# Performance work log

Measured on AMD Instinct MI355X. Metric: run time of the kernel, lower is better.

The kernel has to match this reference:

```python
import jax, jax.numpy as jnp
import numpy as np

SIGMA = 1.0
KSIZE = 5
WEAK = 75.0
STRONG = 255.0
LOW_T = 0.00392
HIGH_T = 0.15

# scipy.signal.gaussian(M, std): unnormalized gaussian window
_n = np.arange(KSIZE, dtype=np.float32) - (KSIZE - 1) / 2.0
_g = np.exp(-0.5 * (_n / SIGMA) ** 2).astype(np.float32)
GAUSS_H = jnp.asarray(_g.reshape(1, 1, 1, KSIZE))  # horizontal 1xK
GAUSS_V = jnp.asarray(_g.reshape(1, 1, KSIZE, 1))  # vertical Kx1

_sobel = np.array([[1, 0, -1], [2, 0, -2], [1, 0, -1]], dtype=np.float32)
SOBEL_H = jnp.asarray(_sobel.reshape(1, 1, 3, 3))
SOBEL_V = jnp.asarray(_sobel.T.reshape(1, 1, 3, 3))

_f0 = np.array([[0, 0, 0], [0, 1, -1], [0, 0, 0]], np.float32)
_f45 = np.array([[0, 0, 0], [0, 1, 0], [0, 0, -1]], np.float32)
_f90 = np.array([[0, 0, 0], [0, 1, 0], [0, -1, 0]], np.float32)
_f135 = np.array([[0, 0, 0], [0, 1, 0], [-1, 0, 0]], np.float32)
_f180 = np.array([[0, 0, 0], [-1, 1, 0], [0, 0, 0]], np.float32)
_f225 = np.array([[-1, 0, 0], [0, 1, 0], [0, 0, 0]], np.float32)
_f270 = np.array([[0, -1, 0], [0, 1, 0], [0, 0, 0]], np.float32)
_f315 = np.array([[0, 0, -1], [0, 1, 0], [0, 0, 0]], np.float32)
DIR_FILT = jnp.asarray(np.stack([_f0, _f45, _f90, _f135, _f180, _f225, _f270, _f315]).reshape(8, 1, 3, 3))

NBR_FILT = jnp.asarray(np.array([[1, 1, 1], [1, 0, 1], [1, 1, 1]], np.float32).reshape(1, 1, 3, 3))


def _conv(x, w, pad):
    # cross-correlation, matching torch F.conv2d
    return jax.lax.conv_general_dilated(
        x, w, window_strides=(1, 1), padding=[(pad[0], pad[0]), (pad[1], pad[1])],
        dimension_numbers=('NCHW', 'OIHW', 'NCHW'))


def setup_inputs() -> dict:
    key = jax.random.key(0)
    img = jax.random.uniform(key, (16, 1, 1024, 1024), dtype=jnp.float32)
    return {"img": img}


def reference(img):
    B = img.shape[0]
    # --- gaussian noise removal (separable) ---
    sm = _conv(img, GAUSS_H, (0, KSIZE // 2))
    sm = _conv(sm, GAUSS_V, (KSIZE // 2, 0))
    # --- sobel gradients ---
    Ix = _conv(sm, SOBEL_H, (1, 1))
    Iy = _conv(sm, SOBEL_V, (1, 1))
    mag = jnp.sqrt(Ix ** 2 + Iy ** 2)
    mag = mag / mag.reshape(B, -1).max(axis=1).reshape(B, 1, 1, 1)
    direction = jnp.arctan2(Iy, Ix) * (180.0 / 3.1415926) + 180.0
    direction = jnp.round(direction / 45.0) * 45.0
    # --- non-max suppression via directional differences + gather ---
    all_filtered = _conv(mag, DIR_FILT, (1, 1))  # [B,8,H,W]
    idx_pos = (direction / 45.0).astype(jnp.int32) % 8  # [B,1,H,W]
    idx_neg = (idx_pos + 4) % 8
    cs_pos = jnp.take_along_axis(all_filtered, idx_pos, axis=1)
    cs_neg = jnp.take_along_axis(all_filtered, idx_neg, axis=1)
    is_max = jnp.minimum(cs_pos, cs_neg) > 0.0
    thin = jnp.where(is_max, mag, 0.0)
    # --- double threshold ---
    hi = thin.max() * HIGH_T  # global max, as in source
    strong = thin >= hi
    weak = (thin < hi) & (thin >= LOW_T)
    inter = jnp.where(strong, STRONG, jnp.where(weak, WEAK, 0.0))
    # --- hysteresis: iterate until no weak pixel gains a strong neighbor ---
    def cond(state):
        return state[1]

    def body(state):
        x, _ = state
        weak_m = x == WEAK
        sn = _conv((x == STRONG).astype(jnp.float32), NBR_FILT, (1, 1))
        new_strong = weak_m & (sn > 0.0)
        x = jnp.where(new_strong, STRONG, x)
        return x, new_strong.any()

    final, _ = jax.lax.while_loop(cond, body, (inter, jnp.asarray(True)))
    final = jnp.where(final == STRONG, final, 0.0)
    return final
```

## Files before the change

### kernel.cpp

```cpp
#include <hip/hip_runtime.h>
#include <math.h>

#define BB 16
#define H 1024
#define W 1024
#define HW (H*W)
#define NTOT (BB*HW)

typedef unsigned long long u64;

__device__ __constant__ float GW[5] = {
    0.13533528323661270f, 0.60653065971263342f, 1.0f,
    0.60653065971263342f, 0.13533528323661270f};

__device__ __constant__ int NBDY[8] = {0, 1, 1, 1, 0, -1, -1, -1};
__device__ __constant__ int NBDX[8] = {1, 1, 0, -1, -1, -1, 0, 1};

#define CSCALE ((float)(180.0 / 3.1415926))

#define TW 128
#define TH 8
__global__ __launch_bounds__(256, 8) void k_smooth_sobel(const float* __restrict__ img,
                                                         float* __restrict__ mag,
                                                         unsigned char* __restrict__ bucket,
                                                         float* __restrict__ partial) {
#pragma clang fp contract(off)
    __shared__ float sA[14 * 136 + 16];
    __shared__ float sB[14 * 132];
    __shared__ float red[256];

    const int tid = threadIdx.x;
    const int x0 = blockIdx.x * TW;
    const int y0 = blockIdx.y * TH;
    const int b = blockIdx.z;
    const size_t base = (size_t)b * HW;

    for (int idx = tid; idx < 14 * 34; idx += 256) {
        int r = idx / 34, v = idx - r * 34;
        int gy = y0 - 3 + r;
        int gxv = x0 - 4 + v * 4;
        float4 val = make_float4(0.f, 0.f, 0.f, 0.f);
        if (gy >= 0 && gy < H && gxv >= 0 && gxv <= W - 4)
            val = *(const float4*)&img[base + (size_t)gy * W + gxv];
        *(float4*)&sA[r * 136 + v * 4] = val;
    }
    __syncthreads();

    for (int idx = tid; idx < 14 * 33; idx += 256) {
        int r = idx / 33, g = idx - r * 33;
        const float* p = &sA[r * 136 + g * 4];
        float4 A0 = *(const float4*)p;
        float4 A1 = *(const float4*)(p + 4);
        float4 A2 = *(const float4*)(p + 8);
        float a_[12] = {A0.x, A0.y, A0.z, A0.w, A1.x, A1.y, A1.z, A1.w,
                        A2.x, A2.y, A2.z, A2.w};
        float o[4];
#pragma unroll
        for (int j = 0; j < 4; ++j) {
            float s = 0.0f;
#pragma unroll
            for (int k = 0; k < 5; ++k) s = s + GW[k] * a_[j + 1 + k];
            o[j] = s;
        }
        *(float4*)&sB[r * 132 + g * 4] = make_float4(o[0], o[1], o[2], o[3]);
    }
    __syncthreads();

    for (int idx = tid; idx < 10 * 33; idx += 256) {
        int rr = idx / 33, g = idx - rr * 33;
        float bb[20];
#pragma unroll
        for (int k = 0; k < 5; ++k) {
            float4 t = *(const float4*)&sB[(rr + k) * 132 + g * 4];
            bb[k * 4 + 0] = t.x; bb[k * 4 + 1] = t.y;
            bb[k * 4 + 2] = t.z; bb[k * 4 + 3] = t.w;
        }
        int gy = y0 - 1 + rr;
        bool rowok = (gy >= 0 && gy < H);
        float o[4];
#pragma unroll
        for (int j = 0; j < 4; ++j) {
            float s = 0.0f;
#pragma unroll
            for (int k = 0; k < 5; ++k) s = s + GW[k] * bb[k * 4 + j];
            int gx = x0 - 1 + g * 4 + j;
            o[j] = (rowok && gx >= 0 && gx < W) ? s : 0.0f;
        }
        *(float4*)&sA[rr * 136 + g * 4] = make_float4(o[0], o[1], o[2], o[3]);
    }
    __syncthreads();

    const int r = tid >> 5;
    const int cg = (tid & 31) * 4;
    const int y = y0 + r;
    const float* P0 = &sA[r * 136 + cg];
    const float* P1 = P0 + 136;
    const float* P2 = P1 + 136;
    float4 q0 = *(const float4*)P0; float2 e0 = *(const float2*)(P0 + 4);
    float4 q1 = *(const float4*)P1; float2 e1 = *(const float2*)(P1 + 4);
    float4 q2 = *(const float4*)P2; float2 e2 = *(const float2*)(P2 + 4);
    float r0[6] = {q0.x, q0.y, q0.z, q0.w, e0.x, e0.y};
    float r1[6] = {q1.x, q1.y, q1.z, q1.w, e1.x, e1.y};
    float r2[6] = {q2.x, q2.y, q2.z, q2.w, e2.x, e2.y};

    float tmax = 0.0f;
    float mg[4];
    unsigned int bk = 0;
#pragma unroll
    for (int j = 0; j < 4; ++j) {
        float a00 = r0[j], a01 = r0[j + 1], a02 = r0[j + 2];
        float a10 = r1[j],                  a12 = r1[j + 2];
        float a20 = r2[j], a21 = r2[j + 1], a22 = r2[j + 2];

        float Ix = a00;
        Ix = Ix - a02;
        Ix = Ix + 2.0f * a10;
        Ix = Ix - 2.0f * a12;
        Ix = Ix + a20;
        Ix = Ix - a22;

        float Iy = a00;
        Iy = Iy + 2.0f * a01;
        Iy = Iy + a02;
        Iy = Iy - a20;
        Iy = Iy - 2.0f * a21;
        Iy = Iy - a22;

        float t1 = Ix * Ix;
        float t2 = Iy * Iy;
        float m = sqrtf(t1 + t2);
        mg[j] = m;
        tmax = fmaxf(tmax, m);

        float ax = fabsf(Ix), ay = fabsf(Iy);
        float mn = fminf(ax, ay), mx = fmaxf(ax, ay);
        float cr = mn * 0.92387953f - mx * 0.38268343f;
        int bidx;
        if (fabsf(cr) < mx * 3e-5f) {
            float fa2 = (float)atan2((double)Iy, (double)Ix);
            float d2 = fa2 * CSCALE;
            d2 = d2 + 180.0f;
            float t2d = d2 / 45.0f;
            float rr2 = rintf(t2d);
            bidx = ((int)rr2) & 7;
        } else if (ay <= ax * 0.41421356f) {
            bidx = signbit(Ix) ? 0 : 4;
        } else if (ay >= ax * 2.41421356f) {
            bidx = (Iy >= 0.0f) ? 6 : 2;
        } else {
            bidx = (Iy >= 0.0f) ? ((Ix >= 0.0f) ? 5 : 7)
                                : ((Ix >= 0.0f) ? 3 : 1);
        }
        bk |= ((unsigned int)bidx) << (8 * j);
    }
    *(float4*)&mag[base + (size_t)y * W + x0 + cg] = make_float4(mg[0], mg[1], mg[2], mg[3]);
    *(unsigned int*)&bucket[base + (size_t)y * W + x0 + cg] = bk;

    red[tid] = tmax;
    __syncthreads();
    for (int s = 128; s > 0; s >>= 1) {
        if (tid < s) red[tid] = fmaxf(red[tid], red[tid + s]);
        __syncthreads();
    }
    if (tid == 0) {
        int pb = (blockIdx.z * 128 + blockIdx.y) * 8 + blockIdx.x;
        partial[pb] = red[0];
    }
}

__global__ __launch_bounds__(256) void k_redmax_img(const float* __restrict__ partial,
                                                    float* __restrict__ magmax) {
    __shared__ float red[256];
    const float* p = partial + blockIdx.x * 1024;
    float m = 0.0f;
    for (int k = threadIdx.x; k < 1024; k += 256) m = fmaxf(m, p[k]);
    red[threadIdx.x] = m;
    __syncthreads();
    for (int s = 128; s > 0; s >>= 1) {
        if (threadIdx.x < s) red[threadIdx.x] = fmaxf(red[threadIdx.x], red[threadIdx.x + s]);
        __syncthreads();
    }
    if (threadIdx.x == 0) magmax[blockIdx.x] = red[0];
}

__global__ __launch_bounds__(256, 6) void k_nms_b(const float* __restrict__ mag,
                                                  const unsigned char* __restrict__ bucket,
                                                  const float* __restrict__ magmax,
                                                  u64* __restrict__ Mb,
                                                  float* __restrict__ partial) {
#pragma clang fp contract(off)
    __shared__ float sN[34 * 136];
    __shared__ unsigned int nib32[256];
    __shared__ float red[256];

    const int tid = threadIdx.x;
    const int x0 = blockIdx.x * 128;
    const int y0 = blockIdx.y * 32;
    const int b = blockIdx.z;
    const size_t base = (size_t)b * HW;
    const float M = magmax[b];

    for (int idx = tid; idx < 34 * 34; idx += 256) {
        int r = idx / 34, v = idx - r * 34;
        int gy = y0 - 1 + r;
        int gxv = x0 - 4 + v * 4;
        float4 val = make_float4(0.f, 0.f, 0.f, 0.f);
        if (gy >= 0 && gy < H && gxv >= 0 && gxv <= W - 4)
            val = *(const float4*)&mag[base + (size_t)gy * W + gxv];
        *(float4*)&sN[r * 136 + v * 4] = val;
    }
    __syncthreads();

    const int r = tid >> 5;
    const int cg = (tid & 31) * 4;
    float amax = 0.0f;

    for (int k4 = 0; k4 < 4; ++k4) {
        const int rr = k4 * 8 + r;
        const int y = y0 + rr;
        unsigned int bk4 = *(const unsigned int*)&bucket[base + (size_t)y * W + x0 + cg];
        float4 a4 = *(const float4*)&sN[(rr + 1) * 136 + cg + 4];
        float av[4] = {a4.x, a4.y, a4.z, a4.w};
        bool im[4];
        bool bad = false;
        float bpv[4], bnv[4];
        bool g1v[4], g2v[4], f1v[4], f2v[4];
#pragma unroll
        for (int j = 0; j < 4; ++j) {
            int c = cg + j;
            int bkt = (bk4 >> (8 * j)) & 0xff;
            int dy = NBDY[bkt], dx = NBDX[bkt];
            float a = av[j];
            float bp = sN[(rr + 1 + dy) * 136 + c + 4 + dx];
            float bn = sN[(rr + 1 - dy) * 136 + c + 4 - dx];
            bpv[j] = bp; bnv[j] = bn;
            bool g1 = a > bp, g2 = a > bn;
            bool f1 = a >= bp * 1.0000005f;
            bool f2 = a >= bn * 1.0000005f;
            g1v[j] = g1; g2v[j] = g2; f1v[j] = f1; f2v[j] = f2;
            im[j] = g1 && g2;
            bad = bad || (g1 && !f1) || (g2 && !f2);
        }
        if (__any(bad)) {
#pragma unroll
            for (int j = 0; j < 4; ++j) {
                bool b1 = g1v[j] && !f1v[j];
                bool b2 = g2v[j] && !f2v[j];
                if (b1 || b2) {
                    float qa = av[j] / M;
                    bool r1 = g1v[j], r2 = g2v[j];
                    if (b1) r1 = qa > (bpv[j] / M);
                    if (b2) r2 = qa > (bnv[j] / M);
                    im[j] = r1 && r2;
                }
            }
        }
        unsigned int nib = 0;
#pragma unroll
        for (int j = 0; j < 4; ++j) {
            if (im[j]) { nib |= 1u << j; amax = fmaxf(amax, av[j]); }
        }
        nib32[tid] = nib;
        __syncthreads();
        if (tid < 16) {
            int rw = tid >> 1, h = tid & 1;
            u64 w = 0;
#pragma unroll
            for (int j = 0; j < 16; ++j)
                w |= (u64)nib32[rw * 32 + h * 16 + j] << (4 * j);
            int yy = y0 + k4 * 8 + rw;
            int widx = ((b << 8) | ((yy >> 6) << 4) | ((x0 >> 6) + h)) * 64 + (yy & 63);
            Mb[widx] = w;
        }
        __syncthreads();
    }

    red[tid] = amax;
    __syncthreads();
    for (int s = 128; s > 0; s >>= 1) {
        if (tid < s) red[tid] = fmaxf(red[tid], red[tid + s]);
        __syncthreads();
    }
    if (tid == 0)
        partial[(blockIdx.z * 32 + blockIdx.y) * 8 + blockIdx.x] = red[0] / M;
}

__global__ __launch_bounds__(1024) void k_finalize_thr(const float* __restrict__ partial,
                                                       float* __restrict__ hdr,
                                                       float* __restrict__ thr) {
    __shared__ float red[1024];
    float m = 0.0f;
    for (int k = threadIdx.x; k < 4096; k += 1024) m = fmaxf(m, partial[k]);
    red[threadIdx.x] = m;
    __syncthreads();
    for (int s = 512; s > 0; s >>= 1) {
        if (threadIdx.x < s) red[threadIdx.x] = fmaxf(red[threadIdx.x], red[threadIdx.x + s]);
        __syncthreads();
    }
    if (threadIdx.x == 0) hdr[16] = red[0];
    if (threadIdx.x < 32) {
        float tm = red[0];
        int t = threadIdx.x;
        float M = hdr[t >> 1];
        float T = (t & 1) ? (tm * 0.15f) : 0.00392f;
        if (0.0f / M >= T) { thr[t] = 0.0f; return; }
        unsigned int lo = 0u, hi = 0x7f800000u;
        while (hi - lo > 1u) {
            unsigned int mid = lo + ((hi - lo) >> 1);
            if (__uint_as_float(mid) / M >= T) hi = mid; else lo = mid;
        }
        thr[t] = __uint_as_float(hi);
    }
}

__global__ __launch_bounds__(256, 8) void k_thresh_b(const float* __restrict__ mag,
                                                     const u64* __restrict__ Mb,
                                                     const float* __restrict__ hdr,
                                                     const float* __restrict__ thr,
                                                     u64* __restrict__ Sb,
                                                     u64* __restrict__ Wb) {
    __shared__ unsigned int nibS[256], nibW[256];
    const int tid = threadIdx.x;
    const int x0 = blockIdx.x * 128;
    const int y0 = blockIdx.y * 32;
    const int b = blockIdx.z;
    const size_t base = (size_t)b * HW;
    const float Alo = thr[b * 2], Ahi = thr[b * 2 + 1];
    const bool snm = (hdr[16] * 0.15f <= 0.0f);
    const int r = tid >> 5;
    const int cg = (tid & 31) * 4;
    const int hl = cg >> 6;

    for (int k4 = 0; k4 < 4; ++k4) {
        const int rr = k4 * 8 + r;
        const int y = y0 + rr;
        float4 a4 = *(const float4*)&mag[base + (size_t)y * W + x0 + cg];
        float av[4] = {a4.x, a4.y, a4.z, a4.w};
        const int widx = ((b << 8) | ((y >> 6) << 4) | ((x0 >> 6) + hl)) * 64 + (y & 63);
        u64 mw = Mb[widx];
        unsigned int ns = 0, nw = 0;
#pragma unroll
        for (int j = 0; j < 4; ++j) {
            bool im = (mw >> ((cg & 63) + j)) & 1ull;
            bool strong = snm || (im && (av[j] >= Ahi));
            bool weak = (!strong) && im && (av[j] >= Alo);
            ns |= (strong ? 1u : 0u) << j;
            nw |= (weak ? 1u : 0u) << j;
        }
        nibS[tid] = ns;
        nibW[tid] = nw;
        __syncthreads();
        if (tid < 32) {
            bool isW = (tid >= 16);
            int t = tid & 15;
            int rw = t >> 1, h = t & 1;
            const unsigned int* nb = isW ? nibW : nibS;
            u64 w = 0;
#pragma unroll
            for (int j = 0; j < 16; ++j)
                w |= (u64)nb[rw * 32 + h * 16 + j] << (4 * j);
            int yy = y0 + k4 * 8 + rw;
            int widx2 = ((b << 8) | ((yy >> 6) << 4) | ((x0 >> 6) + h)) * 64 + (yy & 63);
            if (isW) Wb[widx2] = w; else Sb[widx2] = w;
        }
        __syncthreads();
    }
}

template <bool LAST>
__global__ __launch_bounds__(256) void k_hyster_bits(const u64* __restrict__ Wb,
                                                     u64* __restrict__ Sb,
                                                     float* __restrict__ out) {
    const int lane = threadIdx.x & 63;
    const int t = blockIdx.x * 4 + (threadIdx.x >> 6);
    const int ty = (t >> 4) & 15;
    const int tx = t & 15;
    const int idx = t * 64 + lane;

    u64 S = Sb[idx];
    const u64 Wk = Wb[idx];

    u64 hstat = 0;
    if (tx > 0)  hstat |= (Sb[(t - 1) * 64 + lane] >> 63) & 1ull;
    if (tx < 15) hstat |= (Sb[(t + 1) * 64 + lane] & 1ull) << 63;

    u64 halo = 0;
    if (lane == 0 && ty > 0) {
        const int ta = t - 16;
        u64 tc = Sb[ta * 64 + 63];
        u64 hh = (tc << 1) | tc | (tc >> 1);
        if (tx > 0)  hh |= (Sb[(ta - 1) * 64 + 63] >> 63) & 1ull;
        if (tx < 15) hh |= (Sb[(ta + 1) * 64 + 63] & 1ull) << 63;
        halo = hh;
    }
    if (lane == 63 && ty < 15) {
        const int tb = t + 16;
        u64 tc = Sb[tb * 64 + 0];
        u64 hh = (tc << 1) | tc | (tc >> 1);
        if (tx > 0)  hh |= (Sb[(tb - 1) * 64 + 0] >> 63) & 1ull;
        if (tx < 15) hh |= (Sb[(tb + 1) * 64 + 0] & 1ull) << 63;
        halo = hh;
    }

    {
        u64 eu = __shfl_up(hstat, 1, 64);
        u64 ed = __shfl_down(hstat, 1, 64);
        if (lane == 0)  eu = halo;
        if (lane == 63) ed = halo;
        S |= Wk & (hstat | eu | ed);
    }

    for (int it = 0; it < 160; ++it) {
        u64 x = S;
        x |= (x << 1) & Wk;
        x |= (x >> 1) & Wk;
        u64 pL = Wk & (Wk << 1);
        u64 pR = Wk & (Wk >> 1);
        x |= (x << 2) & pL;   x |= (x >> 2) & pR;
        pL &= pL << 2;        pR &= pR >> 2;
        x |= (x << 4) & pL;   x |= (x >> 4) & pR;
        pL &= pL << 4;        pR &= pR >> 4;
        x |= (x << 8) & pL;   x |= (x >> 8) & pR;
        pL &= pL << 8;        pR &= pR >> 8;
        x |= (x << 16) & pL;  x |= (x >> 16) & pR;
        pL &= pL << 16;       pR &= pR >> 16;
        x |= (x << 32) & pL;  x |= (x >> 32) & pR;
        u64 hh = x | (x << 1) | (x >> 1);
        u64 up = __shfl_up(hh, 1, 64);
        if (lane == 0) up = 0;
        u64 dn = __shfl_down(hh, 1, 64);
        if (lane == 63) dn = 0;
        u64 nS = x | (Wk & (up | dn));
        bool ch = (nS != S);
        S = nS;
        if (!__any(ch)) break;
    }

    if (!LAST) {
        Sb[idx] = S;
    } else {
        const int bimg = t >> 8;
        float* op = out + (size_t)bimg * HW + (size_t)(ty * 64) * W + tx * 64 + lane;
#pragma unroll 4
        for (int rr = 0; rr < 64; ++rr) {
            u64 wrow = __shfl(S, rr, 64);
            op[(size_t)rr * W] = ((wrow >> lane) & 1ull) ? 255.0f : 0.0f;
        }
    }
}

extern "C" void kernel_launch(void* const* d_in, const int* in_sizes, int n_in,
                              void* d_out, int out_size, void* d_ws, size_t ws_size,
                              hipStream_t stream) {
    (void)in_sizes; (void)n_in; (void)out_size; (void)ws_size;
    const float* img = (const float*)d_in[0];
    float* out = (float*)d_out;

    float* hdr = (float*)d_ws;
    float* thr = hdr + 64;
    float* partialA = hdr + 128;
    float* partialB = partialA + 16384;
    float* A = partialB + 4096;
    unsigned char* C = (unsigned char*)(A + (size_t)NTOT);
    u64* Sb = (u64*)(C + (size_t)NTOT);
    u64* Wb = Sb + NTOT / 64;
    u64* Mb = Wb + NTOT / 64;

    dim3 blk(256);
    k_smooth_sobel<<<dim3(8, 128, BB), blk, 0, stream>>>(img, A, C, partialA);
    k_redmax_img<<<dim3(BB), blk, 0, stream>>>(partialA, hdr);
    k_nms_b<<<dim3(8, 32, BB), blk, 0, stream>>>(A, C, hdr, Mb, partialB);
    k_finalize_thr<<<dim3(1), dim3(1024), 0, stream>>>(partialB, hdr, thr);
    k_thresh_b<<<dim3(8, 32, BB), blk, 0, stream>>>(A, Mb, hdr, thr, Sb, Wb);
    for (int p = 0; p < 5; ++p)
        k_hyster_bits<false><<<dim3(NTOT / (64 * 64) / 4), blk, 0, stream>>>(Wb, Sb, out);
    k_hyster_bits<true><<<dim3(NTOT / (64 * 64) / 4), blk, 0, stream>>>(Wb, Sb, out);
}
```

Baseline: 247.2 us.

## Add vertical flood pass via in-register 64x64 bit transpose in hysteresis

Each hysteresis iteration now transposes the 64x64 bit tile with warp shuffles, runs the same log-step run flood along the vertical direction, and transposes back. Strong labels can then travel the full height of a tile in one iteration instead of one row per iteration, which should cut the number of iterations needed to converge. The cost is two 6-stage shuffle transposes plus a second flood on every iteration.

```diff
diff --git a/kernel.cpp b/kernel.cpp
--- a/kernel.cpp
+++ b/kernel.cpp
@@ -367,6 +367,46 @@
     }
 }
 
+__device__ __forceinline__ u64 transpose64(u64 x, int lane) {
+    u64 y;
+    y = __shfl_xor(x, 32, 64);
+    x = (lane & 32) ? ((x & 0xFFFFFFFF00000000ull) | ((y >> 32) & 0x00000000FFFFFFFFull))
+                    : ((x & 0x00000000FFFFFFFFull) | ((y << 32) & 0xFFFFFFFF00000000ull));
+    y = __shfl_xor(x, 16, 64);
+    x = (lane & 16) ? ((x & 0xFFFF0000FFFF0000ull) | ((y >> 16) & 0x0000FFFF0000FFFFull))
+                    : ((x & 0x0000FFFF0000FFFFull) | ((y << 16) & 0xFFFF0000FFFF0000ull));
+    y = __shfl_xor(x, 8, 64);
+    x = (lane & 8)  ? ((x & 0xFF00FF00FF00FF00ull) | ((y >> 8)  & 0x00FF00FF00FF00FFull))
+                    : ((x & 0x00FF00FF00FF00FFull) | ((y << 8)  & 0xFF00FF00FF00FF00ull));
+    y = __shfl_xor(x, 4, 64);
+    x = (lane & 4)  ? ((x & 0xF0F0F0F0F0F0F0F0ull) | ((y >> 4)  & 0x0F0F0F0F0F0F0F0Full))
+                    : ((x & 0x0F0F0F0F0F0F0F0Full) | ((y << 4)  & 0xF0F0F0F0F0F0F0F0ull));
+    y = __shfl_xor(x, 2, 64);
+    x = (lane & 2)  ? ((x & 0xCCCCCCCCCCCCCCCCull) | ((y >> 2)  & 0x3333333333333333ull))
+                    : ((x & 0x3333333333333333ull) | ((y << 2)  & 0xCCCCCCCCCCCCCCCCull));
+    y = __shfl_xor(x, 1, 64);
+    x = (lane & 1)  ? ((x & 0xAAAAAAAAAAAAAAAAull) | ((y >> 1)  & 0x5555555555555555ull))
+                    : ((x & 0x5555555555555555ull) | ((y << 1)  & 0xAAAAAAAAAAAAAAAAull));
+    return x;
+}
+
+__device__ __forceinline__ u64 hflood(u64 x, u64 Wk) {
+    x |= (x << 1) & Wk;
+    x |= (x >> 1) & Wk;
+    u64 pL = Wk & (Wk << 1);
+    u64 pR = Wk & (Wk >> 1);
+    x |= (x << 2) & pL;   x |= (x >> 2) & pR;
+    pL &= pL << 2;        pR &= pR >> 2;
+    x |= (x << 4) & pL;   x |= (x >> 4) & pR;
+    pL &= pL << 4;        pR &= pR >> 4;
+    x |= (x << 8) & pL;   x |= (x >> 8) & pR;
+    pL &= pL << 8;        pR &= pR >> 8;
+    x |= (x << 16) & pL;  x |= (x >> 16) & pR;
+    pL &= pL << 16;       pR &= pR >> 16;
+    x |= (x << 32) & pL;  x |= (x >> 32) & pR;
+    return x;
+}
+
 template <bool LAST>
 __global__ __launch_bounds__(256) void k_hyster_bits(const u64* __restrict__ Wb,
                                                      u64* __restrict__ Sb,
@@ -410,29 +450,22 @@
         S |= Wk & (hstat | eu | ed);
     }
 
+    const u64 WkT = transpose64(Wk, lane);
+
     for (int it = 0; it < 160; ++it) {
-        u64 x = S;
-        x |= (x << 1) & Wk;
-        x |= (x >> 1) & Wk;
-        u64 pL = Wk & (Wk << 1);
-        u64 pR = Wk & (Wk >> 1);
-        x |= (x << 2) & pL;   x |= (x >> 2) & pR;
-        pL &= pL << 2;        pR &= pR >> 2;
-        x |= (x << 4) & pL;   x |= (x >> 4) & pR;
-        pL &= pL << 4;        pR &= pR >> 4;
-        x |= (x << 8) & pL;   x |= (x >> 8) & pR;
-        pL &= pL << 8;        pR &= pR >> 8;
-        x |= (x << 16) & pL;  x |= (x >> 16) & pR;
-        pL &= pL << 16;       pR &= pR >> 16;
-        x |= (x << 32) & pL;  x |= (x >> 32) & pR;
+        u64 x = hflood(S, Wk);
         u64 hh = x | (x << 1) | (x >> 1);
         u64 up = __shfl_up(hh, 1, 64);
         if (lane == 0) up = 0;
         u64 dn = __shfl_down(hh, 1, 64);
         if (lane == 63) dn = 0;
-        u64 nS = x | (Wk & (up | dn));
-        bool ch = (nS != S);
-        S = nS;
+        x |= Wk & (up | dn);
+        u64 xt = transpose64(x, lane);
+        xt = hflood(xt, WkT);
+        x = transpose64(xt, lane);
+
+        bool ch = (x != S);
+        S = x;
         if (!__any(ch)) break;
     }
 
```

After: 272.4 us. 10.2% more time.
